# Kernel optimization log

Measured on AMD Instinct MI355X. Metric: run time of the kernel, lower is better.

Reference implementation:

```python
import jax, jax.numpy as jnp
import numpy as np

# ---- hierarchy: 6 parents (0..5), 20 leaves (6..25) ----
N_CLASSES = 26
IGNORE = 26
EPS = 1e-8
FACTOR = 5.0
N_PARENTS = 6
PARENTS = np.arange(N_PARENTS)
LEAVES = np.arange(6, 26)
LEAF_PARENT = np.array([0, 0, 0, 1, 1, 1, 2, 2, 2, 3, 3, 3, 4, 4, 4, 5, 5, 5, 5, 5])

# hier_tree[c, p] = 1 iff p == c or p is an ancestor of c
_hier = np.eye(N_CLASSES, dtype=np.float32)
_hier[LEAVES, LEAF_PARENT] = 1.0
HIER_TREE = jnp.asarray(_hier)


def setup_inputs() -> dict:
    key = jax.random.key(0)
    k1, k2 = jax.random.split(key)
    logits = jax.random.normal(k1, (4, N_CLASSES, 512, 512), dtype=jnp.float32)
    # labels in [0, 27): 0..25 real classes, 26 == ignore label
    labels = jax.random.randint(k2, (4, 512, 512), 0, 27)
    return {"logits": logits, "labels": labels}


def _hiera_loss(logits, labels):
    probs = jax.nn.sigmoid(logits)  # [B,C,H,W]
    valid = (labels != IGNORE)[:, None, :, :]  # [B,1,H,W]

    # one-hot with ignore -> all-zero rows for void pixels (label==26 matches nothing)
    onehot = (labels[:, None, :, :] == jnp.arange(N_CLASSES)[None, :, None, None]).astype(probs.dtype)
    # propagate leaf label up to all ancestors: [B,C,H,W]
    labels_all = jnp.einsum('bchw,cp->bphw', onehot, HIER_TREE)

    # ---- deepest level (leaves): no descendants -> MCMA = prob; one ancestor -> MCLA = min(self, parent)
    mcma_leaf = probs[:, LEAVES]  # [B,20,H,W]
    mcla_leaf = jnp.minimum(mcma_leaf, probs[:, LEAF_PARENT])
    lab_leaf = labels_all[:, LEAVES]

    # ---- top level (parents): MCMA = max(self, descendants); no ancestors -> MCLA = prob
    child = jnp.transpose(probs[:, LEAVES], (1, 0, 2, 3))  # [20,B,H,W]
    child_max = jax.ops.segment_max(child, jnp.asarray(LEAF_PARENT), num_segments=N_PARENTS)
    child_max = jnp.transpose(child_max, (1, 0, 2, 3))  # [B,6,H,W]
    mcma_par = jnp.maximum(probs[:, PARENTS], child_max)
    mcla_par = probs[:, PARENTS]
    lab_par = labels_all[:, PARENTS]

    validf = valid.astype(probs.dtype)
    num_valid = validf.sum()

    loss = jnp.zeros((), probs.dtype)
    ce_loss = jnp.zeros((), probs.dtype)
    # level order in the original: deepest first
    for mcma, mcla, lab in ((mcma_leaf, mcla_leaf, lab_leaf), (mcma_par, mcla_par, lab_par)):
        k = mcma.shape[1]
        bce = (-lab * jnp.log(mcla + EPS) - (1.0 - lab) * jnp.log(1.0 - mcma + EPS)) * validf
        loss = loss + bce.sum() / num_valid / k
        # nn.CrossEntropyLoss with soft (probability) targets, reduction='mean'
        logp = jax.nn.log_softmax(mcma, axis=1)
        ce_loss = ce_loss + (-(lab * logp).sum(axis=1)).mean()

    return FACTOR * loss + ce_loss


def reference(logits, labels):
    return _hiera_loss(logits, labels)
```

## Files before the change

kernel.cpp:

```cpp
#include <hip/hip_runtime.h>

namespace {

constexpr int HW    = 512 * 512;
constexpr int NBATCH = 4;
constexpr int NPIX  = NBATCH * HW;
constexpr int NCLS  = 26;
constexpr float EPS = 1e-8f;

__global__ __launch_bounds__(64) void hiera_zero(float* __restrict__ acc) {
  if (threadIdx.x < 3) acc[threadIdx.x] = 0.0f;
}

__global__ __launch_bounds__(256) void hiera_main(
    const float* __restrict__ logits, const int* __restrict__ labels,
    float* __restrict__ acc) {
  constexpr int LP[20] = {0,0,0,1,1,1,2,2,2,3,3,3,4,4,4,5,5,5,5,5};

  float a_bce = 0.0f, a_ce = 0.0f, a_vd = 0.0f;
  const int ngroups = NPIX / 4;
  const int stride  = gridDim.x * blockDim.x;

  for (int g = blockIdx.x * blockDim.x + threadIdx.x; g < ngroups; g += stride) {
    const int p0 = g << 2;
    const int b  = p0 / HW;
    const int hw = p0 - b * HW;
    const float* base = logits + (size_t)b * NCLS * HW + hw;

    float4 x[NCLS];
#pragma unroll
    for (int c = 0; c < NCLS; ++c) {
      float4 v = *reinterpret_cast<const float4*>(base + (size_t)c * HW);
      v.x = 1.0f / (1.0f + __expf(-v.x));
      v.y = 1.0f / (1.0f + __expf(-v.y));
      v.z = 1.0f / (1.0f + __expf(-v.z));
      v.w = 1.0f / (1.0f + __expf(-v.w));
      x[c] = v;
    }
    const int4 lb = *reinterpret_cast<const int4*>(labels + p0);

#pragma unroll
    for (int j = 0; j < 4; ++j) {
      const int L = (j == 0) ? lb.x : (j == 1) ? lb.y : (j == 2) ? lb.z : lb.w;
      float pr[NCLS];
#pragma unroll
      for (int c = 0; c < NCLS; ++c)
        pr[c] = (j == 0) ? x[c].x : (j == 1) ? x[c].y : (j == 2) ? x[c].z : x[c].w;

      const bool valid = (L != 26);

      float cmax[6] = {0.f, 0.f, 0.f, 0.f, 0.f, 0.f};
      float bce_l = 0.0f, se_l = 0.0f, sel_l = 0.0f;
      int parL = -1;
#pragma unroll
      for (int i = 0; i < 20; ++i) {
        const int lp = LP[i];
        const float m  = pr[6 + i];
        const float mc = fminf(m, pr[lp]);
        cmax[lp] = fmaxf(cmax[lp], m);
        const bool lab = (L == 6 + i);
        bce_l -= __logf(lab ? (mc + EPS) : (1.0f - m + EPS));
        se_l  += __expf(m);
        sel_l  = lab ? m : sel_l;
        parL   = lab ? lp : parL;
      }
      const float lse_l = __logf(se_l);

      float bce_p = 0.0f, se_p = 0.0f, sel_p = 0.0f;
#pragma unroll
      for (int p = 0; p < 6; ++p) {
        const float mm = fmaxf(pr[p], cmax[p]);
        const bool lab = (L == p) || (parL == p);
        bce_p -= __logf(lab ? (pr[p] + EPS) : (1.0f - mm + EPS));
        se_p  += __expf(mm);
        sel_p  = lab ? mm : sel_p;
      }
      const float lse_p = __logf(se_p);

      if (valid) {
        a_vd  += 1.0f;
        a_bce += bce_l * (1.0f / 20.0f) + bce_p * (1.0f / 6.0f);
        a_ce  += lse_p - sel_p;
        if (L >= 6) a_ce += lse_l - sel_l;
      }
    }
  }

  const int lane = threadIdx.x & 63;
  const int wid  = threadIdx.x >> 6;
#pragma unroll
  for (int off = 32; off > 0; off >>= 1) {
    a_bce += __shfl_down(a_bce, off);
    a_ce  += __shfl_down(a_ce,  off);
    a_vd  += __shfl_down(a_vd,  off);
  }
  __shared__ float sred[3][4];
  if (lane == 0) { sred[0][wid] = a_bce; sred[1][wid] = a_ce; sred[2][wid] = a_vd; }
  __syncthreads();
  if (threadIdx.x == 0) {
    atomicAdd(&acc[0], sred[0][0] + sred[0][1] + sred[0][2] + sred[0][3]);
    atomicAdd(&acc[1], sred[1][0] + sred[1][1] + sred[1][2] + sred[1][3]);
    atomicAdd(&acc[2], sred[2][0] + sred[2][1] + sred[2][2] + sred[2][3]);
  }
}

__global__ __launch_bounds__(64) void hiera_final(const float* __restrict__ acc,
                                                  float* __restrict__ out) {
  if (threadIdx.x == 0) {
    const float loss = acc[0] / acc[2];
    const float ce   = acc[1] * (1.0f / (float)NPIX);
    out[0] = 5.0f * loss + ce;
  }
}

}

extern "C" void kernel_launch(void* const* d_in, const int* in_sizes, int n_in,
                              void* d_out, int out_size, void* d_ws, size_t ws_size,
                              hipStream_t stream) {
  const float* logits = (const float*)d_in[0];
  const int*   labels = (const int*)d_in[1];
  float* acc = (float*)d_ws;
  float* out = (float*)d_out;

  hiera_zero<<<1, 64, 0, stream>>>(acc);
  hiera_main<<<1024, 256, 0, stream>>>(logits, labels, acc);
  hiera_final<<<1, 64, 0, stream>>>(acc, out);
}
```

Baseline: 197.4 us.

## Map one pixel per thread with full grid and scalar loads

Replaces the grid-stride loop, where each thread handled four pixels through float4 loads, with one thread per pixel and a grid sized to cover all pixels. Division by HW becomes shifts, and the sigmoid uses a hardware reciprocal intrinsic instead of a division. The aim is lower register pressure than holding 26 float4 values, which should allow higher occupancy and better latency hiding on this memory-bound kernel. In exchange it issues more, smaller loads and makes 4096 blocks each do an atomic add instead of 1024.

```diff
diff --git a/kernel.cpp b/kernel.cpp
--- a/kernel.cpp
+++ b/kernel.cpp
@@ -2,11 +2,11 @@
 
 namespace {
 
-constexpr int HW    = 512 * 512;
+constexpr int HW     = 512 * 512;
 constexpr int NBATCH = 4;
-constexpr int NPIX  = NBATCH * HW;
-constexpr int NCLS  = 26;
-constexpr float EPS = 1e-8f;
+constexpr int NPIX   = NBATCH * HW;
+constexpr int NCLS   = 26;
+constexpr float EPS  = 1e-8f;
 
 __global__ __launch_bounds__(64) void hiera_zero(float* __restrict__ acc) {
   if (threadIdx.x < 3) acc[threadIdx.x] = 0.0f;
@@ -17,73 +17,54 @@
     float* __restrict__ acc) {
   constexpr int LP[20] = {0,0,0,1,1,1,2,2,2,3,3,3,4,4,4,5,5,5,5,5};
 
+  const int p  = blockIdx.x * blockDim.x + threadIdx.x;
+  const int b  = p >> 18;
+  const int hw = p & (HW - 1);
+  const float* base = logits + ((size_t)b * NCLS << 18) + hw;
+
+  float pr[NCLS];
+#pragma unroll
+  for (int c = 0; c < NCLS; ++c) {
+    const float x = base[(size_t)c << 18];
+    pr[c] = __builtin_amdgcn_rcpf(1.0f + __expf(-x));
+  }
+  const int L = labels[p];
+  const bool valid = (L != 26);
+
+  float cmax[6] = {0.f, 0.f, 0.f, 0.f, 0.f, 0.f};
+  float bce_l = 0.0f, se_l = 0.0f, sel_l = 0.0f;
+  int parL = -1;
+#pragma unroll
+  for (int i = 0; i < 20; ++i) {
+    const int lp = LP[i];
+    const float m  = pr[6 + i];
+    const float mc = fminf(m, pr[lp]);
+    cmax[lp] = fmaxf(cmax[lp], m);
+    const bool lab = (L == 6 + i);
+    bce_l -= __logf(lab ? (mc + EPS) : (1.0f - m + EPS));
+    se_l  += __expf(m);
+    sel_l  = lab ? m : sel_l;
+    parL   = lab ? lp : parL;
+  }
+  const float lse_l = __logf(se_l);
+
+  float bce_p = 0.0f, se_p = 0.0f, sel_p = 0.0f;
+#pragma unroll
+  for (int q = 0; q < 6; ++q) {
+    const float mm = fmaxf(pr[q], cmax[q]);
+    const bool lab = (L == q) || (parL == q);
+    bce_p -= __logf(lab ? (pr[q] + EPS) : (1.0f - mm + EPS));
+    se_p  += __expf(mm);
+    sel_p  = lab ? mm : sel_p;
+  }
+  const float lse_p = __logf(se_p);
+
   float a_bce = 0.0f, a_ce = 0.0f, a_vd = 0.0f;
-  const int ngroups = NPIX / 4;
-  const int stride  = gridDim.x * blockDim.x;
-
-  for (int g = blockIdx.x * blockDim.x + threadIdx.x; g < ngroups; g += stride) {
-    const int p0 = g << 2;
-    const int b  = p0 / HW;
-    const int hw = p0 - b * HW;
-    const float* base = logits + (size_t)b * NCLS * HW + hw;
-
-    float4 x[NCLS];
-#pragma unroll
-    for (int c = 0; c < NCLS; ++c) {
-      float4 v = *reinterpret_cast<const float4*>(base + (size_t)c * HW);
-      v.x = 1.0f / (1.0f + __expf(-v.x));
-      v.y = 1.0f / (1.0f + __expf(-v.y));
-      v.z = 1.0f / (1.0f + __expf(-v.z));
-      v.w = 1.0f / (1.0f + __expf(-v.w));
-      x[c] = v;
-    }
-    const int4 lb = *reinterpret_cast<const int4*>(labels + p0);
-
-#pragma unroll
-    for (int j = 0; j < 4; ++j) {
-      const int L = (j == 0) ? lb.x : (j == 1) ? lb.y : (j == 2) ? lb.z : lb.w;
-      float pr[NCLS];
-#pragma unroll
-      for (int c = 0; c < NCLS; ++c)
-        pr[c] = (j == 0) ? x[c].x : (j == 1) ? x[c].y : (j == 2) ? x[c].z : x[c].w;
-
-      const bool valid = (L != 26);
-
-      float cmax[6] = {0.f, 0.f, 0.f, 0.f, 0.f, 0.f};
-      float bce_l = 0.0f, se_l = 0.0f, sel_l = 0.0f;
-      int parL = -1;
-#pragma unroll
-      for (int i = 0; i < 20; ++i) {
-        const int lp = LP[i];
-        const float m  = pr[6 + i];
-        const float mc = fminf(m, pr[lp]);
-        cmax[lp] = fmaxf(cmax[lp], m);
-        const bool lab = (L == 6 + i);
-        bce_l -= __logf(lab ? (mc + EPS) : (1.0f - m + EPS));
-        se_l  += __expf(m);
-        sel_l  = lab ? m : sel_l;
-        parL   = lab ? lp : parL;
-      }
-      const float lse_l = __logf(se_l);
-
-      float bce_p = 0.0f, se_p = 0.0f, sel_p = 0.0f;
-#pragma unroll
-      for (int p = 0; p < 6; ++p) {
-        const float mm = fmaxf(pr[p], cmax[p]);
-        const bool lab = (L == p) || (parL == p);
-        bce_p -= __logf(lab ? (pr[p] + EPS) : (1.0f - mm + EPS));
-        se_p  += __expf(mm);
-        sel_p  = lab ? mm : sel_p;
-      }
-      const float lse_p = __logf(se_p);
-
-      if (valid) {
-        a_vd  += 1.0f;
-        a_bce += bce_l * (1.0f / 20.0f) + bce_p * (1.0f / 6.0f);
-        a_ce  += lse_p - sel_p;
-        if (L >= 6) a_ce += lse_l - sel_l;
-      }
-    }
+  if (valid) {
+    a_vd  = 1.0f;
+    a_bce = bce_l * (1.0f / 20.0f) + bce_p * (1.0f / 6.0f);
+    a_ce  = lse_p - sel_p;
+    if (L >= 6) a_ce += lse_l - sel_l;
   }
 
   const int lane = threadIdx.x & 63;
@@ -124,6 +105,6 @@
   float* out = (float*)d_out;
 
   hiera_zero<<<1, 64, 0, stream>>>(acc);
-  hiera_main<<<1024, 256, 0, stream>>>(logits, labels, acc);
+  hiera_main<<<NPIX / 256, 256, 0, stream>>>(logits, labels, acc);
   hiera_final<<<1, 64, 0, stream>>>(acc, out);
 }
```

Result: slower. 295.1 us (+49.5%).
